# Performance work log

Hardware: AMD Instinct MI355X
Metric: run time of the kernel (lower is better)

The kernel has to match this reference:

```python
import jax, jax.numpy as jnp
import numpy as np

E = 256        # HP.EMBED_SIZE
R = 8          # number of derivation rules / MLPs
S = 512        # number of sequential derivation steps
N = 256        # nodes produced per step
N_INIT = 1024  # initial axiom (thax) embeddings
TOTAL = N_INIT + S * N  # 132096 rows in the vectors buffer
M = 65536      # masked nodes fed to eval_net


def setup_inputs() -> dict:
    key = jax.random.key(0)
    ks = jax.random.split(key, 12)
    rng = np.random.default_rng(0)

    init_vecs = jax.random.normal(ks[0], (N_INIT, E), jnp.float32)
    # rule MLPs: concat(2 parents) -> E (relu) -> E
    W1 = jax.random.normal(ks[1], (R, 2 * E, E), jnp.float32) * (1.0 / np.sqrt(2 * E))
    b1 = jnp.zeros((R, E), jnp.float32)
    W2 = jax.random.normal(ks[2], (R, E, E), jnp.float32) * (1.0 / np.sqrt(E))
    b2 = jnp.zeros((R, E), jnp.float32)
    # eval net: E -> E (relu) -> 1
    eval_W1 = jax.random.normal(ks[3], (E, E), jnp.float32) * (1.0 / np.sqrt(E))
    eval_b1 = jnp.zeros((E,), jnp.float32)
    eval_W2 = jax.random.normal(ks[4], (E, 1), jnp.float32) * (1.0 / np.sqrt(E))
    eval_b2 = jnp.zeros((1,), jnp.float32)

    # step s writes rows [N_INIT + s*N, N_INIT + (s+1)*N)
    ind_steps = (N_INIT + np.arange(S * N, dtype=np.int32)).reshape(S, N)
    # parents drawn causally from already-computed prefix [0, N_INIT + s*N)
    highs = (N_INIT + np.arange(S, dtype=np.int64) * N)[:, None, None]
    pars_ind_steps = (rng.random((S, N, 2)) * highs).astype(np.int32)
    rule_steps = rng.integers(0, R, size=(S,)).astype(np.int32)
    mask = rng.integers(0, TOTAL, size=(M,)).astype(np.int32)

    pos = jax.random.uniform(ks[5], (M,), jnp.float32)
    neg = jax.random.uniform(ks[6], (M,), jnp.float32)
    target = jnp.round(jax.random.uniform(ks[7], (M,), jnp.float32))

    return {
        'init_vecs': init_vecs, 'W1': W1, 'b1': b1, 'W2': W2, 'b2': b2,
        'eval_W1': eval_W1, 'eval_b1': eval_b1, 'eval_W2': eval_W2, 'eval_b2': eval_b2,
        'pos': pos, 'neg': neg, 'target': target,
        'ind_steps': jnp.asarray(ind_steps), 'pars_ind_steps': jnp.asarray(pars_ind_steps),
        'rule_steps': jnp.asarray(rule_steps), 'mask': jnp.asarray(mask),
    }


def reference(init_vecs, W1, b1, W2, b2, eval_W1, eval_b1, eval_W2, eval_b2,
              pos, neg, target, ind_steps, pars_ind_steps, rule_steps, mask):
    vectors = jnp.zeros((TOTAL, E), init_vecs.dtype).at[:N_INIT].set(init_vecs)

    def step(vec, xs):
        inds, pars, r = xs            # [N], [N,2], scalar rule id
        p = vec[pars].reshape(N, 2 * E)   # gather parents
        h = jax.nn.relu(p @ W1[r] + b1[r])
        out = h @ W2[r] + b2[r]
        return vec.at[inds].set(out), None  # scatter new node embeddings

    vectors, _ = jax.lax.scan(step, vectors, (ind_steps, pars_ind_steps, rule_steps))

    x = vectors[mask]
    val = (jax.nn.relu(x @ eval_W1 + eval_b1) @ eval_W2 + eval_b2)[:, 0]

    # pos_weight = POS_WEIGHT_EXTRA * tot_neg / tot_pos (constant w.r.t. grads)
    pw = jax.lax.stop_gradient(jnp.sum(neg) / jnp.maximum(jnp.sum(pos), 1.0))
    # BCEWithLogitsLoss(pos_weight, reduction='none')
    contrib = pw * target * jax.nn.softplus(-val) + (1.0 - target) * jax.nn.softplus(val)
    loss = jnp.sum((pos + neg) * contrib)
    posOK = jnp.sum(pos * (val >= 0))
    negOK = jnp.sum(neg * (val < 0))
    return loss, posOK, negOK
```

## Files before the change

kernel.cpp:

```cpp
#include <hip/hip_runtime.h>
#include <math.h>

#define EMB   256
#define TWOE  512
#define NINIT 1024
#define NSTEP 512
#define NPS   256
#define TOTAL (NINIT + NSTEP * NPS)
#define MM    65536
#define NNODE (NSTEP * NPS)
#define NKEY  2048
#define BTH   512
#define TROWS 32
#define CHK_SH  16384
#define RULE_SH (24 * CHK_SH)

typedef short s16x8 __attribute__((ext_vector_type(8)));
typedef float f32x4 __attribute__((ext_vector_type(4)));

#define OFF_VECH   0ull
#define OFF_VECL   ((size_t)TOTAL * EMB * 2)
#define OFF_VAL    (2ull * (size_t)TOTAL * EMB * 2)
#define OFF_CNT    (OFF_VAL + (size_t)MM * 4)
#define OFF_ACC    (OFF_CNT + 4096)
#define OFF_KCNT   (OFF_ACC + 256)
#define OFF_KOFS   (OFF_KCNT + (size_t)NKEY * 4)
#define OFF_NL     (OFF_KOFS + (size_t)NKEY * 4)
#define OFF_TPL    (OFF_NL + 256)
#define OFF_BROWS  (OFF_TPL + 4096)
#define OFF_WSPLIT (OFF_BROWS + (size_t)NNODE * 4)


__device__ __forceinline__ void store_dev_u32(unsigned* p, unsigned v) {
  asm volatile("global_store_dword %0, %1, off sc0 sc1" :: "v"(p), "v"(v) : "memory");
}
__device__ __forceinline__ void store_dev_b64(void* p, uint2 v) {
  asm volatile("global_store_dwordx2 %0, %1, off sc0 sc1" :: "v"(p), "v"(v) : "memory");
}
__device__ __forceinline__ void store_dev_b128(void* p, uint4 v) {
  store_dev_b64(p, make_uint2(v.x, v.y));
  store_dev_b64((char*)p + 8, make_uint2(v.z, v.w));
}
__device__ __forceinline__ unsigned load_dev_u32(const unsigned* p) {
  unsigned r;
  asm volatile("global_load_dword %0, %1, off sc0 sc1\n\ts_waitcnt vmcnt(0)"
               : "=v"(r) : "v"(p) : "memory");
  return r;
}

__device__ __forceinline__ void split8(const float* f, uint4& h4, uint4& l4) {
  unsigned hu[8], lu[8];
  #pragma unroll
  for (int i = 0; i < 8; ++i) {
    unsigned u = __builtin_bit_cast(unsigned, f[i]);
    float rh = __builtin_bit_cast(float, u & 0xffff0000u);
    float rl = f[i] - rh;
    hu[i] = u >> 16;
    lu[i] = __builtin_bit_cast(unsigned, rl) >> 16;
  }
  h4 = make_uint4(hu[0] | (hu[1] << 16), hu[2] | (hu[3] << 16),
                  hu[4] | (hu[5] << 16), hu[6] | (hu[7] << 16));
  l4 = make_uint4(lu[0] | (lu[1] << 16), lu[2] | (lu[3] << 16),
                  lu[4] | (lu[5] << 16), lu[6] | (lu[7] << 16));
}
__device__ __forceinline__ void split1(float f, short& hi, short& lo) {
  unsigned u = __builtin_bit_cast(unsigned, f);
  float rh = __builtin_bit_cast(float, u & 0xffff0000u);
  float rl = f - rh;
  hi = (short)(u >> 16);
  lo = (short)(__builtin_bit_cast(unsigned, rl) >> 16);
}

__global__ void zero_scratch(unsigned* done, double* acc) {
  if (threadIdx.x < 256) done[threadIdx.x] = 0u;
  if (threadIdx.x < 8) acc[threadIdx.x] = 0.0;
}

__global__ void init_convert(const float* __restrict__ src,
                             unsigned short* __restrict__ vh,
                             unsigned short* __restrict__ vl) {
  int slot = blockIdx.x * blockDim.x + threadIdx.x;
  float f[8];
  *(float4*)&f[0] = reinterpret_cast<const float4*>(src)[slot * 2];
  *(float4*)&f[4] = reinterpret_cast<const float4*>(src)[slot * 2 + 1];
  uint4 h4, l4;
  split8(f, h4, l4);
  *(uint4*)(vh + (size_t)slot * 8) = h4;
  *(uint4*)(vl + (size_t)slot * 8) = l4;
}

__global__ __launch_bounds__(512)
void presplit(const float* __restrict__ W1, const float* __restrict__ W2,
              short* __restrict__ Ws)
{
  const int blk = blockIdx.x;
  const int r = blk / 24, c = blk % 24;
  const float* src; int kbase;
  if (c < 16) { src = W1 + (size_t)r * TWOE * EMB; kbase = c * 32; }
  else        { src = W2 + (size_t)r * EMB * EMB;  kbase = (c - 16) * 32; }
  short* dst = Ws + (size_t)blk * CHK_SH;
  const int tid = threadIdx.x;
  #pragma unroll
  for (int u = 0; u < 2; ++u) {
    int qq = tid + u * 512;
    int g = qq >> 6, l = qq & 63;
    const float* p = src + (size_t)(kbase + ((l >> 4) << 3)) * EMB + (g << 4) + (l & 15);
    float f[8];
    #pragma unroll
    for (int i = 0; i < 8; ++i) f[i] = p[i * EMB];
    uint4 h4, l4;
    split8(f, h4, l4);
    *(uint4*)(dst + (size_t)qq * 8) = h4;
    *(uint4*)(dst + 8192 + (size_t)qq * 8) = l4;
  }
}

__global__ __launch_bounds__(1024)
void prepass(const int* __restrict__ pars, const int* __restrict__ rules,
             int* __restrict__ kcnt, int* __restrict__ kofs,
             int* __restrict__ brows, int* __restrict__ tpl, int* __restrict__ nlp)
{
  __shared__ unsigned char slvl[TOTAL];
  __shared__ int scnt[NKEY];
  __shared__ int sofs[NKEY];
  __shared__ int swmax[16];
  const int t = threadIdx.x;
  for (int i = t; i < NINIT; i += 1024) slvl[i] = 0;
  for (int k = t; k < NKEY; k += 1024) scnt[k] = 0;
  __syncthreads();
  int Pa[8], Pb[8];
  if (t < NPS) {
    #pragma unroll
    for (int w = 0; w < 8; ++w) {
      Pa[w] = pars[2 * (w * NPS + t)];
      Pb[w] = pars[2 * (w * NPS + t) + 1];
    }
  }
  int lmax = 0;
  for (int s0 = 0; s0 < NSTEP; s0 += 8) {
    int Na[8], Nb[8];
    if (t < NPS && s0 + 8 < NSTEP) {
      #pragma unroll
      for (int w = 0; w < 8; ++w) {
        Na[w] = pars[2 * ((s0 + 8 + w) * NPS + t)];
        Nb[w] = pars[2 * ((s0 + 8 + w) * NPS + t) + 1];
      }
    }
    #pragma unroll
    for (int w = 0; w < 8; ++w) {
      if (t < NPS) {
        int l1 = slvl[Pa[w]], l2 = slvl[Pb[w]];
        int lv = 1 + (l1 > l2 ? l1 : l2);
        slvl[NINIT + (s0 + w) * NPS + t] = (unsigned char)lv;
        if (lv > lmax) lmax = lv;
      }
      __syncthreads();
    }
    if (t < NPS && s0 + 8 < NSTEP) {
      #pragma unroll
      for (int w = 0; w < 8; ++w) { Pa[w] = Na[w]; Pb[w] = Nb[w]; }
    }
  }
  for (int o = 32; o; o >>= 1) lmax = max(lmax, __shfl_down(lmax, o));
  if ((t & 63) == 0) swmax[t >> 6] = lmax;
  __syncthreads();
  if (t == 0) {
    int m = 0;
    for (int w = 0; w < 16; ++w) m = max(m, swmax[w]);
    nlp[0] = m;
  }
  for (int i = t; i < NNODE; i += 1024) {
    int key = (int)slvl[NINIT + i] * 8 + rules[i >> 8];
    atomicAdd(&scnt[key], 1);
  }
  __syncthreads();
  if (t == 0) {
    int run = 0;
    for (int k = 0; k < NKEY; ++k) {
      sofs[k] = run; kofs[k] = run; kcnt[k] = scnt[k]; run += scnt[k];
    }
  }
  __syncthreads();
  if (t < 256) {
    int s = 0;
    #pragma unroll
    for (int r = 0; r < 8; ++r) s += (scnt[t * 8 + r] + TROWS - 1) >> 5;
    tpl[t] = s;
  }
  for (int i = t; i < NNODE; i += 1024) {
    int key = (int)slvl[NINIT + i] * 8 + rules[i >> 8];
    int pos = atomicAdd(&sofs[key], 1);
    brows[pos] = i;
  }
}

__global__ __launch_bounds__(BTH, 1)
void scan_kernel(const short* __restrict__ Ws, const float* __restrict__ b1,
                 const float* __restrict__ b2, const int* __restrict__ pars,
                 unsigned short* __restrict__ vech, unsigned short* __restrict__ vecl,
                 const int* __restrict__ kcnt, const int* __restrict__ kofs,
                 const int* __restrict__ brows, const int* __restrict__ tpl,
                 const int* __restrict__ nlp, unsigned* __restrict__ done)
{
  __shared__ short wB[2][CHK_SH];
  __shared__ short hH[TROWS][264];
  __shared__ short hLo[TROWS][264];
  __shared__ int spar[2 * TROWS];
  __shared__ int sorow[TROWS];
  const int tid = threadIdx.x;
  const int bid = blockIdx.x;
  const int lane = tid & 63;
  const int w = tid >> 6;
  const int rw = w & 1, cwb = (w >> 1) << 2;
  const int row16 = lane & 15, kb8 = (lane >> 4) << 3;
  const int arow = (rw << 4) + row16;
  const int hrow = (rw << 4) + ((lane >> 4) << 2);
  const int NL = nlp[0];
  const int xcd = bid & 7, jb = bid >> 3;

  for (int lv = 1; lv <= NL; ++lv) {
    if (tid == 0 && lv > 1) {
      const unsigned need = (unsigned)tpl[lv - 1];
      const unsigned* dp = done + (lv - 1);
      while (load_dev_u32(dp) < need) __builtin_amdgcn_s_sleep(2);
    }
    __syncthreads();
    int cum[9]; cum[0] = 0;
    int cnts[8], ofss[8];
    #pragma unroll
    for (int r = 0; r < 8; ++r) {
      int c = kcnt[lv * 8 + r];
      cnts[r] = c; ofss[r] = kofs[lv * 8 + r];
      cum[r + 1] = cum[r] + ((c + TROWS - 1) >> 5);
    }
    const int G = cum[8];
    const int q = G >> 3, rm = G & 7;
    const int Gx = q + (xcd < rm ? 1 : 0);
    const int sx = xcd * q + (xcd < rm ? xcd : rm);
    for (int j = jb; j < Gx; j += 32) {
      const int g = sx + j;
      int rr = 0;
      while (g >= cum[rr + 1]) ++rr;
      const int t0 = g - cum[rr];
      const int cnt_b = cnts[rr], ofs_b = ofss[rr];
      const int tbase = t0 * TROWS;
      const short* __restrict__ Wr = Ws + (size_t)rr * RULE_SH;

      __syncthreads();
      if (tid < 2 * TROWS) {
        int slot = tbase + (tid >> 1);
        if (slot >= cnt_b) slot = cnt_b - 1;
        int node = brows[ofs_b + slot];
        spar[tid] = pars[2 * node + (tid & 1)];
        if ((tid & 1) == 0) sorow[tid >> 1] = NINIT + node;
      }
      uint4 st0, st1, st2, st3;
      {
        const short* cs = Wr;
        st0 = *(const uint4*)(cs + (size_t)tid * 8);
        st1 = *(const uint4*)(cs + (size_t)(512 + tid) * 8);
        st2 = *(const uint4*)(cs + 8192 + (size_t)tid * 8);
        st3 = *(const uint4*)(cs + 8192 + (size_t)(512 + tid) * 8);
      }
      __syncthreads();
      const int par0 = spar[2 * arow], par1 = spar[2 * arow + 1];
      float b1v[4], b2v[4];
      #pragma unroll
      for (int g4 = 0; g4 < 4; ++g4) {
        b1v[g4] = b1[rr * EMB + ((cwb + g4) << 4) + row16];
        b2v[g4] = b2[rr * EMB + ((cwb + g4) << 4) + row16];
      }
      uint4 ahA, alA;
      {
        size_t off = (size_t)par0 * EMB + kb8;
        ahA = *(const uint4*)(vech + off);
        alA = *(const uint4*)(vecl + off);
      }
      {
        *(uint4*)&wB[0][tid * 8] = st0;
        *(uint4*)&wB[0][(512 + tid) * 8] = st1;
        *(uint4*)&wB[0][8192 + tid * 8] = st2;
        *(uint4*)&wB[0][8192 + (512 + tid) * 8] = st3;
      }
      __syncthreads();
      f32x4 acc[4] = {{0,0,0,0},{0,0,0,0},{0,0,0,0},{0,0,0,0}};
      int curb = 0;
      for (int c = 0; c < 16; ++c) {
        {
          const short* cs = Wr + (size_t)(c + 1) * CHK_SH;
          st0 = *(const uint4*)(cs + (size_t)tid * 8);
          st1 = *(const uint4*)(cs + (size_t)(512 + tid) * 8);
          st2 = *(const uint4*)(cs + 8192 + (size_t)tid * 8);
          st3 = *(const uint4*)(cs + 8192 + (size_t)(512 + tid) * 8);
        }
        uint4 ahB = ahA, alB = alA;
        if (c < 15) {
          int kg = (c + 1) * 32 + kb8;
          int par = (kg >> 8) ? par1 : par0;
          size_t off = (size_t)par * EMB + (kg & 255);
          ahB = *(const uint4*)(vech + off);
          alB = *(const uint4*)(vecl + off);
        }
        {
          s16x8 Ah = __builtin_bit_cast(s16x8, ahA);
          s16x8 Al = __builtin_bit_cast(s16x8, alA);
          #pragma unroll
          for (int g4 = 0; g4 < 4; ++g4) {
            int gi = (cwb + g4) * 64 + lane;
            s16x8 Bh = *(const s16x8*)&wB[curb][gi * 8];
            s16x8 Bl = *(const s16x8*)&wB[curb][8192 + gi * 8];
            acc[g4] = __builtin_amdgcn_mfma_f32_16x16x32_bf16(Ah, Bh, acc[g4], 0, 0, 0);
            acc[g4] = __builtin_amdgcn_mfma_f32_16x16x32_bf16(Ah, Bl, acc[g4], 0, 0, 0);
            acc[g4] = __builtin_amdgcn_mfma_f32_16x16x32_bf16(Al, Bh, acc[g4], 0, 0, 0);
          }
        }
        if (c == 15) {
          #pragma unroll
          for (int g4 = 0; g4 < 4; ++g4) {
            #pragma unroll
            for (int jj = 0; jj < 4; ++jj) {
              int col = ((cwb + g4) << 4) + row16;
              short hi, lo;
              split1(fmaxf(acc[g4][jj] + b1v[g4], 0.f), hi, lo);
              hH[hrow + jj][col] = hi; hLo[hrow + jj][col] = lo;
            }
          }
        }
        {
          *(uint4*)&wB[curb ^ 1][tid * 8] = st0;
          *(uint4*)&wB[curb ^ 1][(512 + tid) * 8] = st1;
          *(uint4*)&wB[curb ^ 1][8192 + tid * 8] = st2;
          *(uint4*)&wB[curb ^ 1][8192 + (512 + tid) * 8] = st3;
        }
        __syncthreads();
        curb ^= 1;
        ahA = ahB; alA = alB;
      }
      f32x4 acc2[4] = {{0,0,0,0},{0,0,0,0},{0,0,0,0},{0,0,0,0}};
      for (int c2 = 0; c2 < 8; ++c2) {
        if (c2 < 7) {
          const short* cs = Wr + (size_t)(17 + c2) * CHK_SH;
          st0 = *(const uint4*)(cs + (size_t)tid * 8);
          st1 = *(const uint4*)(cs + (size_t)(512 + tid) * 8);
          st2 = *(const uint4*)(cs + 8192 + (size_t)tid * 8);
          st3 = *(const uint4*)(cs + 8192 + (size_t)(512 + tid) * 8);
        }
        const int kc = c2 * 32 + kb8;
        s16x8 Ah = *(const s16x8*)&hH[arow][kc];
        s16x8 Al = *(const s16x8*)&hLo[arow][kc];
        #pragma unroll
        for (int g4 = 0; g4 < 4; ++g4) {
          int gi = (cwb + g4) * 64 + lane;
          s16x8 Bh = *(const s16x8*)&wB[curb][gi * 8];
          s16x8 Bl = *(const s16x8*)&wB[curb][8192 + gi * 8];
          acc2[g4] = __builtin_amdgcn_mfma_f32_16x16x32_bf16(Ah, Bh, acc2[g4], 0, 0, 0);
          acc2[g4] = __builtin_amdgcn_mfma_f32_16x16x32_bf16(Ah, Bl, acc2[g4], 0, 0, 0);
          acc2[g4] = __builtin_amdgcn_mfma_f32_16x16x32_bf16(Al, Bh, acc2[g4], 0, 0, 0);
        }
        if (c2 < 7) {
          *(uint4*)&wB[curb ^ 1][tid * 8] = st0;
          *(uint4*)&wB[curb ^ 1][(512 + tid) * 8] = st1;
          *(uint4*)&wB[curb ^ 1][8192 + tid * 8] = st2;
          *(uint4*)&wB[curb ^ 1][8192 + (512 + tid) * 8] = st3;
          __syncthreads();
          curb ^= 1;
        }
      }
      __syncthreads();
      #pragma unroll
      for (int g4 = 0; g4 < 4; ++g4) {
        #pragma unroll
        for (int jj = 0; jj < 4; ++jj) {
          int col = ((cwb + g4) << 4) + row16;
          short hi, lo;
          split1(acc2[g4][jj] + b2v[g4], hi, lo);
          hH[hrow + jj][col] = hi; hLo[hrow + jj][col] = lo;
        }
      }
      __syncthreads();
      #pragma unroll
      for (int u = 0; u < 2; ++u) {
        int s = tid + u * 512;
        int row = s >> 5, c8 = (s & 31) * 8;
        uint4 h4 = *(const uint4*)&hH[row][c8];
        uint4 l4 = *(const uint4*)&hLo[row][c8];
        if (tbase + row < cnt_b) {
          size_t off = (size_t)sorow[row] * EMB + c8;
          store_dev_b128(vech + off, h4);
          store_dev_b128(vecl + off, l4);
        }
      }
      asm volatile("s_waitcnt vmcnt(0)" ::: "memory");
      __syncthreads();
      if (tid == 0)
        __hip_atomic_fetch_add(done + lv, 1u, __ATOMIC_RELAXED, __HIP_MEMORY_SCOPE_AGENT);
    }
  }
}

__global__ void reduce_pn(const float* __restrict__ pos, const float* __restrict__ neg,
                          double* acc) {
  double sp = 0.0, sn = 0.0;
  for (int m = blockIdx.x * blockDim.x + threadIdx.x; m < MM; m += gridDim.x * blockDim.x) {
    sp += (double)pos[m]; sn += (double)neg[m];
  }
  for (int o = 32; o; o >>= 1) { sp += __shfl_down(sp, o); sn += __shfl_down(sn, o); }
  __shared__ double rp[4], rn[4];
  int wid = threadIdx.x >> 6, lane = threadIdx.x & 63;
  if (lane == 0) { rp[wid] = sp; rn[wid] = sn; }
  __syncthreads();
  if (threadIdx.x == 0) {
    double tp = 0.0, tn = 0.0;
    for (int w = 0; w < 4; ++w) { tp += rp[w]; tn += rn[w]; }
    atomicAdd(&acc[0], tp); atomicAdd(&acc[1], tn);
  }
}

__global__ __launch_bounds__(256)
void eval_kernel(const unsigned short* __restrict__ vh, const unsigned short* __restrict__ vl,
                 const int* __restrict__ mask,
                 const float* __restrict__ eW1, const float* __restrict__ eb1,
                 const float* __restrict__ eW2, const float* __restrict__ eb2,
                 float* __restrict__ val)
{
  __shared__ float xL[64][36];
  __shared__ float wLx[32][260];
  __shared__ int mrow[64];
  const int tid = threadIdx.x;
  const int a = tid >> 4, b = tid & 15;
  const int m0 = blockIdx.x * 64;
  if (tid < 64) mrow[tid] = mask[m0 + tid];
  __syncthreads();

  float acc[4][16];
  #pragma unroll
  for (int i = 0; i < 4; ++i)
    #pragma unroll
    for (int j = 0; j < 16; ++j) acc[i][j] = 0.f;

  for (int c = 0; c < 8; ++c) {
    const int e0 = c * 32;
    for (int idx = tid; idx < 64 * 4; idx += 256) {
      int rr = idx >> 2, u = idx & 3;
      size_t off = (size_t)mrow[rr] * EMB + e0 + u * 8;
      uint4 hv = *(const uint4*)(vh + off);
      uint4 lv = *(const uint4*)(vl + off);
      const unsigned* hu = (const unsigned*)&hv;
      const unsigned* lu = (const unsigned*)&lv;
      float fo[8];
      #pragma unroll
      for (int jj = 0; jj < 4; ++jj) {
        fo[2 * jj] = __builtin_bit_cast(float, (hu[jj] & 0xffffu) << 16) +
                     __builtin_bit_cast(float, (lu[jj] & 0xffffu) << 16);
        fo[2 * jj + 1] = __builtin_bit_cast(float, hu[jj] & 0xffff0000u) +
                         __builtin_bit_cast(float, lu[jj] & 0xffff0000u);
      }
      *(float4*)&xL[rr][u * 8] = *(float4*)&fo[0];
      *(float4*)&xL[rr][u * 8 + 4] = *(float4*)&fo[4];
    }
    for (int idx = tid; idx < 32 * 64; idx += 256) {
      int e = idx >> 6, k4 = idx & 63;
      reinterpret_cast<float4*>(&wLx[e][0])[k4] =
          reinterpret_cast<const float4*>(eW1 + (size_t)(e0 + e) * EMB)[k4];
    }
    __syncthreads();
    #pragma unroll 4
    for (int e = 0; e < 32; ++e) {
      float xs[4];
      #pragma unroll
      for (int rr = 0; rr < 4; ++rr) xs[rr] = xL[a * 4 + rr][e];
      const float4* wr = reinterpret_cast<const float4*>(&wLx[e][0]) + b * 4;
      float wk[16];
      *reinterpret_cast<float4*>(&wk[0])  = wr[0];
      *reinterpret_cast<float4*>(&wk[4])  = wr[1];
      *reinterpret_cast<float4*>(&wk[8])  = wr[2];
      *reinterpret_cast<float4*>(&wk[12]) = wr[3];
      #pragma unroll
      for (int rr = 0; rr < 4; ++rr)
        #pragma unroll
        for (int kk = 0; kk < 16; ++kk)
          acc[rr][kk] = fmaf(xs[rr], wk[kk], acc[rr][kk]);
    }
    __syncthreads();
  }

  float eb2v = eb2[0];
  float pv[4];
  #pragma unroll
  for (int rr = 0; rr < 4; ++rr) {
    float s = 0.f;
    #pragma unroll
    for (int kk = 0; kk < 16; ++kk) {
      float h = acc[rr][kk] + eb1[b * 16 + kk];
      h = fmaxf(h, 0.f);
      s += h * eW2[b * 16 + kk];
    }
    pv[rr] = s;
  }
  #pragma unroll
  for (int m = 1; m < 16; m <<= 1) {
    #pragma unroll
    for (int rr = 0; rr < 4; ++rr) pv[rr] += __shfl_xor(pv[rr], m);
  }
  if (b == 0) {
    #pragma unroll
    for (int rr = 0; rr < 4; ++rr) val[m0 + a * 4 + rr] = pv[rr] + eb2v;
  }
}

__global__ void loss_kernel(const float* __restrict__ val, const float* __restrict__ pos,
                            const float* __restrict__ neg, const float* __restrict__ tgt,
                            double* acc)
{
  const float pw = (float)(acc[1] / fmax(acc[0], 1.0));
  double l = 0.0, pk = 0.0, nk = 0.0;
  for (int m = blockIdx.x * blockDim.x + threadIdx.x; m < MM; m += gridDim.x * blockDim.x) {
    float v = val[m], p = pos[m], n = neg[m], t = tgt[m];
    float lp = log1pf(expf(-fabsf(v)));
    float spn = fmaxf(-v, 0.f) + lp;
    float spp = fmaxf(v, 0.f) + lp;
    float contrib = pw * t * spn + (1.f - t) * spp;
    l += (double)((p + n) * contrib);
    if (v >= 0.f) pk += (double)p; else nk += (double)n;
  }
  for (int o = 32; o; o >>= 1) {
    l += __shfl_down(l, o); pk += __shfl_down(pk, o); nk += __shfl_down(nk, o);
  }
  __shared__ double s0[4], s1[4], s2[4];
  int wid = threadIdx.x >> 6, lane = threadIdx.x & 63;
  if (lane == 0) { s0[wid] = l; s1[wid] = pk; s2[wid] = nk; }
  __syncthreads();
  if (threadIdx.x == 0) {
    double ta = 0.0, tb = 0.0, tc = 0.0;
    for (int w = 0; w < 4; ++w) { ta += s0[w]; tb += s1[w]; tc += s2[w]; }
    atomicAdd(&acc[2], ta); atomicAdd(&acc[3], tb); atomicAdd(&acc[4], tc);
  }
}

__global__ void writeout(const double* __restrict__ acc, float* __restrict__ out) {
  if (threadIdx.x == 0) {
    out[0] = (float)acc[2];
    out[1] = (float)acc[3];
    out[2] = (float)acc[4];
  }
}

extern "C" void kernel_launch(void* const* d_in, const int* in_sizes, int n_in,
                              void* d_out, int out_size, void* d_ws, size_t ws_size,
                              hipStream_t stream)
{
  (void)in_sizes; (void)n_in; (void)out_size; (void)ws_size;
  const float* init_vecs = (const float*)d_in[0];
  const float* W1  = (const float*)d_in[1];
  const float* b1  = (const float*)d_in[2];
  const float* W2  = (const float*)d_in[3];
  const float* b2  = (const float*)d_in[4];
  const float* eW1 = (const float*)d_in[5];
  const float* eb1 = (const float*)d_in[6];
  const float* eW2 = (const float*)d_in[7];
  const float* eb2 = (const float*)d_in[8];
  const float* pos = (const float*)d_in[9];
  const float* neg = (const float*)d_in[10];
  const float* tgt = (const float*)d_in[11];
  const int* pars  = (const int*)d_in[13];
  const int* rules = (const int*)d_in[14];
  const int* mask  = (const int*)d_in[15];

  char* ws = (char*)d_ws;
  unsigned short* vech = (unsigned short*)(ws + OFF_VECH);
  unsigned short* vecl = (unsigned short*)(ws + OFF_VECL);
  float*    val   = (float*)(ws + OFF_VAL);
  unsigned* done  = (unsigned*)(ws + OFF_CNT);
  double*   acc   = (double*)(ws + OFF_ACC);
  int*      kcnt  = (int*)(ws + OFF_KCNT);
  int*      kofs  = (int*)(ws + OFF_KOFS);
  int*      nlp   = (int*)(ws + OFF_NL);
  int*      tpl   = (int*)(ws + OFF_TPL);
  int*      brows = (int*)(ws + OFF_BROWS);
  short*    Ws    = (short*)(ws + OFF_WSPLIT);

  zero_scratch<<<1, 256, 0, stream>>>(done, acc);
  prepass<<<1, 1024, 0, stream>>>(pars, rules, kcnt, kofs, brows, tpl, nlp);
  init_convert<<<128, 256, 0, stream>>>(init_vecs, vech, vecl);
  presplit<<<192, 512, 0, stream>>>(W1, W2, Ws);
  scan_kernel<<<256, BTH, 0, stream>>>(Ws, b1, b2, pars, vech, vecl,
                                       kcnt, kofs, brows, tpl, nlp, done);
  reduce_pn<<<128, 256, 0, stream>>>(pos, neg, acc);
  eval_kernel<<<1024, 256, 0, stream>>>(vech, vecl, mask, eW1, eb1, eW2, eb2, val);
  loss_kernel<<<128, 256, 0, stream>>>(val, pos, neg, tgt, acc);
  writeout<<<1, 1, 0, stream>>>(acc, (float*)d_out);
}
```

Measured before the change: 1.221 ms.

## Deepen weight and parent prefetch pipeline in fully unrolled fused MLP loop

Merges the two MLP layer loops into one fully unrolled 24-chunk loop. Weight chunks are now prefetched two chunks ahead through two register sets, and parent activations three chunks ahead through a three-slot register ring. The aim is to hide global-load latency behind the MFMA work and drop the extra barrier between the two layers. The cost is more VGPR pressure from the extra prefetch registers and larger code from full unrolling, which could cause spills.

Result: faster. 1.115 ms, median of 2 (-8.7%).

```diff
diff --git a/kernel.cpp b/kernel.cpp
--- a/kernel.cpp
+++ b/kernel.cpp
@@ -193,6 +193,18 @@
     brows[pos] = i;
   }
 }
+
+#define LOADW(S0, S1, S2, S3, ch) { \
+  const short* cs_ = Wr + (size_t)(ch) * CHK_SH; \
+  S0 = *(const uint4*)(cs_ + (size_t)tid * 8); \
+  S1 = *(const uint4*)(cs_ + (size_t)(512 + tid) * 8); \
+  S2 = *(const uint4*)(cs_ + 8192 + (size_t)tid * 8); \
+  S3 = *(const uint4*)(cs_ + 8192 + (size_t)(512 + tid) * 8); }
+#define WRITEW(buf, S0, S1, S2, S3) { \
+  *(uint4*)&wB[buf][tid * 8] = S0; \
+  *(uint4*)&wB[buf][(512 + tid) * 8] = S1; \
+  *(uint4*)&wB[buf][8192 + tid * 8] = S2; \
+  *(uint4*)&wB[buf][8192 + (512 + tid) * 8] = S3; }
 
 __global__ __launch_bounds__(BTH, 1)
 void scan_kernel(const short* __restrict__ Ws, const float* __restrict__ b1,
@@ -254,14 +266,8 @@
         spar[tid] = pars[2 * node + (tid & 1)];
         if ((tid & 1) == 0) sorow[tid >> 1] = NINIT + node;
       }
-      uint4 st0, st1, st2, st3;
-      {
-        const short* cs = Wr;
-        st0 = *(const uint4*)(cs + (size_t)tid * 8);
-        st1 = *(const uint4*)(cs + (size_t)(512 + tid) * 8);
-        st2 = *(const uint4*)(cs + 8192 + (size_t)tid * 8);
-        st3 = *(const uint4*)(cs + 8192 + (size_t)(512 + tid) * 8);
-      }
+      uint4 sA0, sA1, sA2, sA3, sB0, sB1, sB2, sB3;
+      LOADW(sA0, sA1, sA2, sA3, 0);
       __syncthreads();
       const int par0 = spar[2 * arow], par1 = spar[2 * arow + 1];
       float b1v[4], b2v[4];
@@ -270,51 +276,49 @@
         b1v[g4] = b1[rr * EMB + ((cwb + g4) << 4) + row16];
         b2v[g4] = b2[rr * EMB + ((cwb + g4) << 4) + row16];
       }
-      uint4 ahA, alA;
-      {
-        size_t off = (size_t)par0 * EMB + kb8;
-        ahA = *(const uint4*)(vech + off);
-        alA = *(const uint4*)(vecl + off);
-      }
-      {
-        *(uint4*)&wB[0][tid * 8] = st0;
-        *(uint4*)&wB[0][(512 + tid) * 8] = st1;
-        *(uint4*)&wB[0][8192 + tid * 8] = st2;
-        *(uint4*)&wB[0][8192 + (512 + tid) * 8] = st3;
-      }
+      uint4 ah[3], al[3];
+      #pragma unroll
+      for (int d = 0; d < 3; ++d) {
+        int kg = d * 32 + kb8;
+        int par = (kg >> 8) ? par1 : par0;
+        size_t off = (size_t)par * EMB + (kg & 255);
+        ah[d] = *(const uint4*)(vech + off);
+        al[d] = *(const uint4*)(vecl + off);
+      }
+      WRITEW(0, sA0, sA1, sA2, sA3);
+      LOADW(sB0, sB1, sB2, sB3, 1);
       __syncthreads();
-      f32x4 acc[4] = {{0,0,0,0},{0,0,0,0},{0,0,0,0},{0,0,0,0}};
-      int curb = 0;
-      for (int c = 0; c < 16; ++c) {
-        {
-          const short* cs = Wr + (size_t)(c + 1) * CHK_SH;
-          st0 = *(const uint4*)(cs + (size_t)tid * 8);
-          st1 = *(const uint4*)(cs + (size_t)(512 + tid) * 8);
-          st2 = *(const uint4*)(cs + 8192 + (size_t)tid * 8);
-          st3 = *(const uint4*)(cs + 8192 + (size_t)(512 + tid) * 8);
-        }
-        uint4 ahB = ahA, alB = alA;
-        if (c < 15) {
-          int kg = (c + 1) * 32 + kb8;
-          int par = (kg >> 8) ? par1 : par0;
-          size_t off = (size_t)par * EMB + (kg & 255);
-          ahB = *(const uint4*)(vech + off);
-          alB = *(const uint4*)(vecl + off);
-        }
-        {
-          s16x8 Ah = __builtin_bit_cast(s16x8, ahA);
-          s16x8 Al = __builtin_bit_cast(s16x8, alA);
+      f32x4 acc[4]  = {{0,0,0,0},{0,0,0,0},{0,0,0,0},{0,0,0,0}};
+      f32x4 acc2[4] = {{0,0,0,0},{0,0,0,0},{0,0,0,0},{0,0,0,0}};
+      #pragma unroll
+      for (int cc = 0; cc < 24; ++cc) {
+        if (cc < 16) {
+          s16x8 Ah = __builtin_bit_cast(s16x8, ah[cc % 3]);
+          s16x8 Al = __builtin_bit_cast(s16x8, al[cc % 3]);
           #pragma unroll
           for (int g4 = 0; g4 < 4; ++g4) {
             int gi = (cwb + g4) * 64 + lane;
-            s16x8 Bh = *(const s16x8*)&wB[curb][gi * 8];
-            s16x8 Bl = *(const s16x8*)&wB[curb][8192 + gi * 8];
+            s16x8 Bh = *(const s16x8*)&wB[cc & 1][gi * 8];
+            s16x8 Bl = *(const s16x8*)&wB[cc & 1][8192 + gi * 8];
             acc[g4] = __builtin_amdgcn_mfma_f32_16x16x32_bf16(Ah, Bh, acc[g4], 0, 0, 0);
             acc[g4] = __builtin_amdgcn_mfma_f32_16x16x32_bf16(Ah, Bl, acc[g4], 0, 0, 0);
             acc[g4] = __builtin_amdgcn_mfma_f32_16x16x32_bf16(Al, Bh, acc[g4], 0, 0, 0);
           }
-        }
-        if (c == 15) {
+        } else {
+          const int kc = (cc - 16) * 32 + kb8;
+          s16x8 Ah = *(const s16x8*)&hH[arow][kc];
+          s16x8 Al = *(const s16x8*)&hLo[arow][kc];
+          #pragma unroll
+          for (int g4 = 0; g4 < 4; ++g4) {
+            int gi = (cwb + g4) * 64 + lane;
+            s16x8 Bh = *(const s16x8*)&wB[cc & 1][gi * 8];
+            s16x8 Bl = *(const s16x8*)&wB[cc & 1][8192 + gi * 8];
+            acc2[g4] = __builtin_amdgcn_mfma_f32_16x16x32_bf16(Ah, Bh, acc2[g4], 0, 0, 0);
+            acc2[g4] = __builtin_amdgcn_mfma_f32_16x16x32_bf16(Ah, Bl, acc2[g4], 0, 0, 0);
+            acc2[g4] = __builtin_amdgcn_mfma_f32_16x16x32_bf16(Al, Bh, acc2[g4], 0, 0, 0);
+          }
+        }
+        if (cc == 15) {
           #pragma unroll
           for (int g4 = 0; g4 < 4; ++g4) {
             #pragma unroll
@@ -326,47 +330,24 @@
             }
           }
         }
-        {
-          *(uint4*)&wB[curb ^ 1][tid * 8] = st0;
-          *(uint4*)&wB[curb ^ 1][(512 + tid) * 8] = st1;
-          *(uint4*)&wB[curb ^ 1][8192 + tid * 8] = st2;
-          *(uint4*)&wB[curb ^ 1][8192 + (512 + tid) * 8] = st3;
+        if (cc < 23) {
+          if (((cc + 1) & 1) == 0) { WRITEW(0, sA0, sA1, sA2, sA3); }
+          else                     { WRITEW(1, sB0, sB1, sB2, sB3); }
+        }
+        if (cc < 22) {
+          if (((cc + 2) & 1) == 0) { LOADW(sA0, sA1, sA2, sA3, cc + 2); }
+          else                     { LOADW(sB0, sB1, sB2, sB3, cc + 2); }
+        }
+        if (cc + 3 <= 15) {
+          int d = (cc + 3) % 3;
+          int kg = (cc + 3) * 32 + kb8;
+          int par = (kg >> 8) ? par1 : par0;
+          size_t off = (size_t)par * EMB + (kg & 255);
+          ah[d] = *(const uint4*)(vech + off);
+          al[d] = *(const uint4*)(vecl + off);
         }
         __syncthreads();
-        curb ^= 1;
-        ahA = ahB; alA = alB;
-      }
-      f32x4 acc2[4] = {{0,0,0,0},{0,0,0,0},{0,0,0,0},{0,0,0,0}};
-      for (int c2 = 0; c2 < 8; ++c2) {
-        if (c2 < 7) {
-          const short* cs = Wr + (size_t)(17 + c2) * CHK_SH;
-          st0 = *(const uint4*)(cs + (size_t)tid * 8);
-          st1 = *(const uint4*)(cs + (size_t)(512 + tid) * 8);
-          st2 = *(const uint4*)(cs + 8192 + (size_t)tid * 8);
-          st3 = *(const uint4*)(cs + 8192 + (size_t)(512 + tid) * 8);
-        }
-        const int kc = c2 * 32 + kb8;
-        s16x8 Ah = *(const s16x8*)&hH[arow][kc];
-        s16x8 Al = *(const s16x8*)&hLo[arow][kc];
-        #pragma unroll
-        for (int g4 = 0; g4 < 4; ++g4) {
-          int gi = (cwb + g4) * 64 + lane;
-          s16x8 Bh = *(const s16x8*)&wB[curb][gi * 8];
-          s16x8 Bl = *(const s16x8*)&wB[curb][8192 + gi * 8];
-          acc2[g4] = __builtin_amdgcn_mfma_f32_16x16x32_bf16(Ah, Bh, acc2[g4], 0, 0, 0);
-          acc2[g4] = __builtin_amdgcn_mfma_f32_16x16x32_bf16(Ah, Bl, acc2[g4], 0, 0, 0);
-          acc2[g4] = __builtin_amdgcn_mfma_f32_16x16x32_bf16(Al, Bh, acc2[g4], 0, 0, 0);
-        }
-        if (c2 < 7) {
-          *(uint4*)&wB[curb ^ 1][tid * 8] = st0;
-          *(uint4*)&wB[curb ^ 1][(512 + tid) * 8] = st1;
-          *(uint4*)&wB[curb ^ 1][8192 + tid * 8] = st2;
-          *(uint4*)&wB[curb ^ 1][8192 + (512 + tid) * 8] = st3;
-          __syncthreads();
-          curb ^= 1;
-        }
-      }
-      __syncthreads();
+      }
       #pragma unroll
       for (int g4 = 0; g4 < 4; ++g4) {
         #pragma unroll
```
